# Optimization experiments

Measured on AMD Instinct MI355X. Metric: run time of the kernel, lower is better.

## Reference

```python
import jax, jax.numpy as jnp
import numpy as np

V, D, H, HD, L, T, B = 65, 384, 6, 64, 6, 256, 64
EPS = 1e-3  # keras LayerNormalization default epsilon


def setup_inputs() -> dict:
    key = jax.random.key(0)
    ks = jax.random.split(key, 12)
    s = 0.02
    n = lambda k, shp: jax.random.normal(k, shp, dtype=jnp.float32) * s
    return {
        "idx": jax.random.randint(ks[0], (B, T), 0, V),
        "tok_emb": n(ks[1], (V, D)),
        "pos_emb": n(ks[2], (T, D)),
        "Wq": n(ks[3], (L, H, D, HD)),
        "Wk": n(ks[4], (L, H, D, HD)),
        "Wv": n(ks[5], (L, H, D, HD)),
        "Wproj": n(ks[6], (L, D, D)),
        "bproj": jnp.zeros((L, D), jnp.float32),
        "W1": n(ks[7], (L, D, 4 * D)),
        "b1": jnp.zeros((L, 4 * D), jnp.float32),
        "W2": n(ks[8], (L, 4 * D, D)),
        "b2": jnp.zeros((L, D), jnp.float32),
        "ln1_g": jnp.ones((L, D), jnp.float32),
        "ln1_b": jnp.zeros((L, D), jnp.float32),
        "ln2_g": jnp.ones((L, D), jnp.float32),
        "ln2_b": jnp.zeros((L, D), jnp.float32),
        "lnf_g": jnp.ones((D,), jnp.float32),
        "lnf_b": jnp.zeros((D,), jnp.float32),
        "Whead": n(ks[9], (D, V)),
        "bhead": jnp.zeros((V,), jnp.float32),
    }


def _ln(x, g, b):
    m = jnp.mean(x, axis=-1, keepdims=True)
    v = jnp.mean(jnp.square(x - m), axis=-1, keepdims=True)
    return (x - m) * jax.lax.rsqrt(v + EPS) * g + b


def reference(idx, tok_emb, pos_emb, Wq, Wk, Wv, Wproj, bproj, W1, b1, W2, b2,
              ln1_g, ln1_b, ln2_g, ln2_b, lnf_g, lnf_b, Whead, bhead):
    Bn, Tn = idx.shape
    x = tok_emb[idx] + pos_emb[:Tn]  # [B,T,D]
    mask = jnp.tril(jnp.ones((Tn, Tn), dtype=bool))
    scale = jnp.float32(D) ** -0.5  # NOTE: original scales by full C=n_embd, not head_size
    for l in range(L):
        h = _ln(x, ln1_g[l], ln1_b[l])
        q = jnp.einsum('btd,hdk->bhtk', h, Wq[l])
        k = jnp.einsum('btd,hdk->bhtk', h, Wk[l])
        v = jnp.einsum('btd,hdk->bhtk', h, Wv[l])
        wei = jnp.einsum('bhtk,bhsk->bhts', q, k) * scale
        wei = jnp.where(mask, wei, -jnp.inf)
        wei = jax.nn.softmax(wei, axis=-1)
        att = jnp.einsum('bhts,bhsk->bhtk', wei, v)
        att = att.transpose(0, 2, 1, 3).reshape(Bn, Tn, D)  # concat heads
        x = x + att @ Wproj[l] + bproj[l]
        h2 = _ln(x, ln2_g[l], ln2_b[l])
        x = x + jax.nn.relu(h2 @ W1[l] + b1[l]) @ W2[l] + b2[l]
    x = _ln(x, lnf_g, lnf_b)
    return x @ Whead + bhead  # logits [B,T,V]
```

## Files before the change

kernel.cpp:

```cpp
#include <hip/hip_runtime.h>
#include <hip/hip_bf16.h>

#define B_  64
#define T_  256
#define D_  384
#define H_  6
#define HD_ 64
#define L_  6
#define V_  65
#define BT  (B_*T_)

typedef __hip_bfloat16 bf16;
typedef unsigned short u16;
typedef short s16;
typedef __attribute__((ext_vector_type(8))) short bf16x8;
typedef __attribute__((ext_vector_type(4))) float f32x4;

#define OFF_QKV   0
#define OFF_PROJ  442368
#define OFF_W1T   589824
#define OFF_W2T   1179648
#define OFF_BPROJ 1769472
#define OFF_B1    1769856
#define OFF_B2    1771392
#define OFF_LN1G  1771776
#define OFF_LN1B  1772160
#define OFF_LN2G  1772544
#define OFF_LN2B  1772928
#define WBUF_E    1773312
#define HOFF_WHT  0
#define HOFF_BH   24960
#define HOFF_LNFG 25088
#define HOFF_LNFB 25472
#define HBUF_E    25856

__device__ __forceinline__ float u2f(u16 u) {
  union { unsigned i; float f; } c; c.i = ((unsigned)u) << 16; return c.f;
}
__device__ __forceinline__ bf16 f2b(float x) { return __float2bfloat16(x); }
__device__ __forceinline__ float b2f(bf16 x) { return __bfloat162float(x); }
__device__ __forceinline__ u16 f2u(float x) { bf16 h = f2b(x); return *(u16*)&h; }

__device__ __forceinline__ float pload(const void* p, size_t i, bool f32w) {
  return f32w ? ((const float*)p)[i] : u2f(((const u16*)p)[i]);
}

__device__ __forceinline__ void swz(int gid, int ntc, int mtiles,
                                    int& nt, int& mblk) {
  if ((mtiles & 7) == 0) {
    int per = ntc << 3;
    int g   = gid / per;
    int rem = gid - g * per;
    nt   = rem >> 3;
    mblk = (g << 3) + (rem & 7);
  } else {
    nt   = gid / mtiles;
    mblk = gid - nt * mtiles;
  }
}

__global__ __launch_bounds__(256) void detect_kernel(
    const void* p1,  const void* p2,  const void* p3,  const void* p4,
    const void* p5,  const void* p6,  const void* p7,  const void* p8,
    const void* p9,  const void* p10, const void* p11, const void* p12,
    const void* p13, const void* p14, const void* p15, const void* p16,
    const void* p17, const void* p18, const void* p19,
    const int* __restrict__ idx, unsigned* flags)
{
  const void* ps[20] = {nullptr, p1, p2, p3, p4, p5, p6, p7, p8, p9, p10,
                        p11, p12, p13, p14, p15, p16, p17, p18, p19};
  const int esz[20] = {16384, 24960, 98304, 884736, 884736, 884736, 884736,
                       2304, 3538944, 9216, 3538944, 2304, 2304, 2304, 2304,
                       2304, 384, 384, 24960, 65};
  __shared__ int r1[256], r2[256];
  int bid = blockIdx.x, tid = threadIdx.x;
  if (bid == 19) {
    int z = 0;
    for (int m = tid; m < 4096; m += 256) z += (idx[2 * m + 1] == 0) ? 1 : 0;
    r1[tid] = z; __syncthreads();
    for (int s = 128; s > 0; s >>= 1) {
      if (tid < s) r1[tid] += r1[tid + s];
      __syncthreads();
    }
    if (tid == 0) flags[20] = (r1[0] >= 4000) ? 1u : 0u;
    return;
  }
  int j = bid + 1;
  const u16* p = (const u16*)ps[j];
  int ns = esz[j] / 2; if (ns > 1024) ns = 1024;
  int band = 0, nz = 0;
  for (int i = tid; i < ns; i += 256) {
    u16 lo = p[2 * i], hi = p[2 * i + 1];
    int e = (lo >> 7) & 0xFF;
    band += (e >= 100 && e <= 127) ? 1 : 0;
    nz   += (lo | hi) ? 1 : 0;
  }
  r1[tid] = band; r2[tid] = nz; __syncthreads();
  for (int s = 128; s > 0; s >>= 1) {
    if (tid < s) { r1[tid] += r1[tid + s]; r2[tid] += r2[tid + s]; }
    __syncthreads();
  }
  if (tid == 0) flags[j] = (r2[0] > 0 && r1[0] * 2 < ns) ? 1u : 0u;
}

__global__ void const_kernel(float* out, int n, float val) {
  int i = blockIdx.x * 256 + threadIdx.x;
  if (i < n) out[i] = val;
}

__global__ __launch_bounds__(256) void conv_layer(
    const void* Wq, const void* Wk, const void* Wv, const void* Wproj,
    const void* bproj, const void* W1, const void* b1, const void* W2,
    const void* b2, const void* ln1g, const void* ln1b, const void* ln2g,
    const void* ln2b, const unsigned* __restrict__ flags,
    bf16* __restrict__ dst, int l)
{
  int e = blockIdx.x * 256 + threadIdx.x;
  if (e >= WBUF_E) return;
  float v;
  if (e < OFF_PROJ) {
    int math = e / 24576;
    int rem  = e - math * 24576;
    int hd = rem / 384, d = rem - hd * 384;
    int mat = math / 6, hh = math - mat * 6;
    const void* src = (mat == 0 ? Wq : mat == 1 ? Wk : Wv);
    v = pload(src, ((size_t)(l * 6 + hh) * 384 + d) * 64 + hd, flags[3 + mat] != 0);
  } else if (e < OFF_W1T) {
    int e2 = e - OFF_PROJ;
    int n = e2 / 384, d = e2 - n * 384;
    v = pload(Wproj, ((size_t)l * 384 + d) * 384 + n, flags[6] != 0);
  } else if (e < OFF_W2T) {
    int e2 = e - OFF_W1T;
    int n = e2 / 384, d = e2 - n * 384;
    v = pload(W1, ((size_t)l * 384 + d) * 1536 + n, flags[8] != 0);
  } else if (e < OFF_BPROJ) {
    int e2 = e - OFF_W2T;
    int n = e2 / 1536, k = e2 - n * 1536;
    v = pload(W2, ((size_t)l * 1536 + k) * 384 + n, flags[10] != 0);
  } else {
    int e2 = e - OFF_BPROJ;
    if      (e2 < 384)  v = pload(bproj, (size_t)l * 384 + e2, flags[7] != 0);
    else if (e2 < 1920) v = pload(b1, (size_t)l * 1536 + (e2 - 384), flags[9] != 0);
    else if (e2 < 2304) v = pload(b2, (size_t)l * 384 + (e2 - 1920), flags[11] != 0);
    else if (e2 < 2688) v = pload(ln1g, (size_t)l * 384 + (e2 - 2304), flags[12] != 0);
    else if (e2 < 3072) v = pload(ln1b, (size_t)l * 384 + (e2 - 2688), flags[13] != 0);
    else if (e2 < 3456) v = pload(ln2g, (size_t)l * 384 + (e2 - 3072), flags[14] != 0);
    else                v = pload(ln2b, (size_t)l * 384 + (e2 - 3456), flags[15] != 0);
  }
  dst[e] = f2b(v);
}

__global__ __launch_bounds__(256) void conv_head(
    const void* Wh, const void* bh, const void* lnfg, const void* lnfb,
    const unsigned* __restrict__ flags, bf16* __restrict__ dst)
{
  int e = blockIdx.x * 256 + threadIdx.x;
  if (e >= HBUF_E) return;
  float v = 0.f;
  if (e < HOFF_BH) {
    int n = e / 384, d = e - n * 384;
    v = pload(Wh, (size_t)d * 65 + n, flags[18] != 0);
  } else if (e < 25025) {
    v = pload(bh, e - HOFF_BH, flags[19] != 0);
  } else if (e < HOFF_LNFG) {
    v = 0.f;
  } else if (e < HOFF_LNFB) {
    v = pload(lnfg, e - HOFF_LNFG, flags[16] != 0);
  } else {
    v = pload(lnfb, e - HOFF_LNFB, flags[17] != 0);
  }
  dst[e] = f2b(v);
}

__global__ __launch_bounds__(256) void embed_kernel(
    const void* __restrict__ idx, const void* __restrict__ tok,
    const void* __restrict__ pos, bf16* __restrict__ x,
    const unsigned* __restrict__ flags)
{
  int i   = blockIdx.x * 256 + threadIdx.x;
  int tkn = i / D_;
  int d   = i - tkn * D_;
  int t   = tkn & (T_ - 1);
  long long tix;
  if (flags[20]) tix = ((const long long*)idx)[tkn];
  else           tix = ((const int*)idx)[tkn];
  float v = pload(tok, (size_t)tix * D_ + d, flags[1] != 0)
          + pload(pos, (size_t)t * D_ + d, flags[2] != 0);
  x[i] = f2b(v);
}

__global__ __launch_bounds__(256) void lnw_kernel(
    const bf16* __restrict__ x, const u16* __restrict__ g,
    const u16* __restrict__ b, bf16* __restrict__ hc, int tok0)
{
  int w = threadIdx.x >> 6, lane = threadIdx.x & 63;
  int lm = blockIdx.x * 4 + w;
  const bf16* xr = x + (size_t)(tok0 + lm) * D_;
  float v[6]; float s = 0.f;
#pragma unroll
  for (int j = 0; j < 6; j++) { v[j] = b2f(xr[lane + 64 * j]); s += v[j]; }
#pragma unroll
  for (int o = 1; o < 64; o <<= 1) s += __shfl_xor(s, o, 64);
  float mean = s * (1.0f / D_);
  float sq = 0.f;
#pragma unroll
  for (int j = 0; j < 6; j++) { float d0 = v[j] - mean; sq += d0 * d0; }
#pragma unroll
  for (int o = 1; o < 64; o <<= 1) sq += __shfl_xor(sq, o, 64);
  float inv = 1.0f / sqrtf(sq * (1.0f / D_) + 1e-3f);
  bf16* hr = hc + (size_t)lm * D_;
#pragma unroll
  for (int j = 0; j < 6; j++) {
    int d = lane + 64 * j;
    hr[d] = f2b((v[j] - mean) * inv * u2f(g[d]) + u2f(b[d]));
  }
}

#define XS_S 72
#define WT_S 72

template<int RELU, int RESID, int OUTF32, int BIAS>
__device__ __forceinline__ void mgemm_core(
    s16* __restrict__ Xs, s16* __restrict__ Wt,
    const u16* __restrict__ A,
    const u16* __restrict__ WT, const bf16* __restrict__ bias,
    const bf16* __restrict__ resid, void* __restrict__ Cout,
    int ldC, int N, int K, int arow0, int crow0, int n0)
{
  int tid = threadIdx.x;
  int w = tid >> 6, lane = tid & 63;
  int quad = lane >> 4, l15 = lane & 15;
  f32x4 acc[2][4];
#pragma unroll
  for (int i = 0; i < 2; i++)
#pragma unroll
    for (int j = 0; j < 4; j++) acc[i][j] = (f32x4){0.f, 0.f, 0.f, 0.f};

  int xr = tid >> 1, xc = (tid & 1) * 32;
  int wn = tid >> 2, wk = (tid & 3) * 16;
  const u16* Ap0 = A + (size_t)(arow0 + xr) * K + xc;
  bool wvalid = (n0 + wn) < N;
  const u16* Wp0 = WT + (size_t)(wvalid ? (n0 + wn) : 0) * K + wk;

  for (int k0 = 0; k0 < K; k0 += 64) {
    bf16x8 xv[4];
#pragma unroll
    for (int i = 0; i < 4; i++) xv[i] = *(const bf16x8*)(Ap0 + k0 + 8 * i);
    bf16x8 wv[2];
#pragma unroll
    for (int i = 0; i < 2; i++)
      wv[i] = wvalid ? *(const bf16x8*)(Wp0 + k0 + 8 * i)
                     : (bf16x8){0,0,0,0,0,0,0,0};
    __syncthreads();
#pragma unroll
    for (int i = 0; i < 4; i++)
      *(bf16x8*)&Xs[xr * XS_S + xc + 8 * i] = xv[i];
#pragma unroll
    for (int i = 0; i < 2; i++)
      *(bf16x8*)&Wt[wn * WT_S + wk + 8 * i] = wv[i];
    __syncthreads();
#pragma unroll
    for (int kh = 0; kh < 2; kh++) {
      int kk = kh * 32 + quad * 8;
      bf16x8 a0 = *(const bf16x8*)&Xs[(w * 32 + l15) * XS_S + kk];
      bf16x8 a1 = *(const bf16x8*)&Xs[(w * 32 + 16 + l15) * XS_S + kk];
#pragma unroll
      for (int nt = 0; nt < 4; nt++) {
        bf16x8 b = *(const bf16x8*)&Wt[(nt * 16 + l15) * WT_S + kk];
        acc[0][nt] = __builtin_amdgcn_mfma_f32_16x16x32_bf16(a0, b, acc[0][nt], 0, 0, 0);
        acc[1][nt] = __builtin_amdgcn_mfma_f32_16x16x32_bf16(a1, b, acc[1][nt], 0, 0, 0);
      }
    }
  }

#pragma unroll
  for (int sub = 0; sub < 2; sub++)
#pragma unroll
    for (int nt = 0; nt < 4; nt++)
#pragma unroll
      for (int r = 0; r < 4; r++) {
        int m = w * 32 + sub * 16 + quad * 4 + r;
        int n = n0 + nt * 16 + l15;
        if (n < N) {
          float v = acc[sub][nt][r];
          if (BIAS)  v += b2f(bias[n]);
          if (RESID) v += b2f(resid[(size_t)(crow0 + m) * ldC + n]);
          if (RELU)  v = fmaxf(v, 0.f);
          if (OUTF32) ((float*)Cout)[(size_t)(crow0 + m) * ldC + n] = v;
          else        ((bf16*)Cout)[(size_t)(crow0 + m) * ldC + n]  = f2b(v);
        }
      }
}

#define MGEMM_LDS __shared__ s16 Xs[128 * XS_S]; __shared__ s16 Wt[64 * WT_S];

__global__ __launch_bounds__(256) void proj_mfma(
    const bf16* A, const bf16* Wbuf, bf16* x, int tok0, int mtiles)
{
  MGEMM_LDS
  int nt, mblk;
  swz(blockIdx.x, 6, mtiles, nt, mblk);
  int n0 = nt * 64, m0 = mblk * 128;
  mgemm_core<0,1,0,1>(Xs, Wt, (const u16*)A,
                      (const u16*)Wbuf + OFF_PROJ, (const bf16*)Wbuf + OFF_BPROJ,
                      x, x, D_, D_, D_, m0, tok0 + m0, n0);
}

__global__ __launch_bounds__(256) void ffn2_mfma(
    const bf16* midc, const bf16* Wbuf, bf16* x, int tok0, int mtiles)
{
  MGEMM_LDS
  int nt, mblk;
  swz(blockIdx.x, 6, mtiles, nt, mblk);
  int n0 = nt * 64, m0 = mblk * 128;
  mgemm_core<0,1,0,1>(Xs, Wt, (const u16*)midc,
                      (const u16*)Wbuf + OFF_W2T, (const bf16*)Wbuf + OFF_B2,
                      x, x, D_, D_, 4 * D_, m0, tok0 + m0, n0);
}

__global__ __launch_bounds__(256) void head_mfma(
    const bf16* hc, const bf16* Hbuf, float* out, int tok0)
{
  MGEMM_LDS
  int n0 = blockIdx.x * 64, m0 = blockIdx.y * 128;
  mgemm_core<0,0,1,1>(Xs, Wt, (const u16*)hc,
                      (const u16*)Hbuf + HOFF_WHT, (const bf16*)Hbuf + HOFF_BH,
                      nullptr, out, V_, V_, D_, m0, tok0 + m0, n0);
}

template<class Epi>
__device__ __forceinline__ void mg128(
    s16* __restrict__ Xs, s16* __restrict__ Ws,
    const u16* __restrict__ A,
    const u16* __restrict__ WT, int N, int K, int arow0, int n0, Epi epi)
{
  int tid = threadIdx.x;
  int w = tid >> 6, lane = tid & 63;
  int quad = lane >> 4, l15 = lane & 15;
  int wm = (w >> 1) * 64, wn = (w & 1) * 64;
  f32x4 acc[4][4];
#pragma unroll
  for (int i = 0; i < 4; i++)
#pragma unroll
    for (int j = 0; j < 4; j++) acc[i][j] = (f32x4){0.f, 0.f, 0.f, 0.f};

  int sr = tid >> 1, sc = (tid & 1) * 32;
  const u16* Ap0 = A + (size_t)(arow0 + sr) * K + sc;
  bool nv = (n0 + sr) < N;
  const u16* Wp0 = WT + (size_t)(nv ? (n0 + sr) : 0) * K + sc;

  for (int k0 = 0; k0 < K; k0 += 64) {
    bf16x8 xv[4], wv[4];
#pragma unroll
    for (int i = 0; i < 4; i++) xv[i] = *(const bf16x8*)(Ap0 + k0 + 8 * i);
#pragma unroll
    for (int i = 0; i < 4; i++)
      wv[i] = nv ? *(const bf16x8*)(Wp0 + k0 + 8 * i)
                 : (bf16x8){0,0,0,0,0,0,0,0};
    __syncthreads();
#pragma unroll
    for (int i = 0; i < 4; i++) {
      *(bf16x8*)&Xs[sr * 72 + sc + 8 * i] = xv[i];
      *(bf16x8*)&Ws[sr * 72 + sc + 8 * i] = wv[i];
    }
    __syncthreads();
#pragma unroll
    for (int kh = 0; kh < 2; kh++) {
      int kk = kh * 32 + quad * 8;
      bf16x8 am[4], bn[4];
#pragma unroll
      for (int i = 0; i < 4; i++)
        am[i] = *(const bf16x8*)&Xs[(wm + i * 16 + l15) * 72 + kk];
#pragma unroll
      for (int j = 0; j < 4; j++)
        bn[j] = *(const bf16x8*)&Ws[(wn + j * 16 + l15) * 72 + kk];
#pragma unroll
      for (int i = 0; i < 4; i++)
#pragma unroll
        for (int j = 0; j < 4; j++)
          acc[i][j] = __builtin_amdgcn_mfma_f32_16x16x32_bf16(am[i], bn[j], acc[i][j], 0, 0, 0);
    }
  }

#pragma unroll
  for (int i = 0; i < 4; i++)
#pragma unroll
    for (int j = 0; j < 4; j++)
#pragma unroll
      for (int r = 0; r < 4; r++) {
        int m = wm + i * 16 + quad * 4 + r;
        int n = n0 + wn + j * 16 + l15;
        if (n < N) epi(m, n, acc[i][j][r]);
      }
}

#define MG128_LDS __shared__ s16 Xs[128 * 72]; __shared__ s16 Ws[128 * 72];

__global__ __launch_bounds__(256) void qkv128(
    const bf16* hc, const bf16* Wbuf, bf16* qkvc, int MCa, int mtiles)
{
  MG128_LDS
  int nt, mblk;
  swz(blockIdx.x, 9, mtiles, nt, mblk);
  int n0 = nt * 128, mloc0 = mblk * 128;
  auto epi = [&](int m, int n, float v) {
    int mat = n / 384;
    int rem = n - mat * 384;
    int hh = rem >> 6, hd = rem & 63;
    qkvc[(size_t)mat * MCa * D_ + (size_t)hh * MCa * HD_
         + (size_t)(mloc0 + m) * HD_ + hd] = f2b(v);
  };
  mg128(Xs, Ws, (const u16*)hc,
        (const u16*)Wbuf + OFF_QKV, 1152, D_, mloc0, n0, epi);
}

__global__ __launch_bounds__(256) void ffn1_128(
    const bf16* hc, const bf16* Wbuf, bf16* midc, int mtiles)
{
  MG128_LDS
  int nt, mblk;
  swz(blockIdx.x, 12, mtiles, nt, mblk);
  int n0 = nt * 128, m0 = mblk * 128;
  const bf16* bias = (const bf16*)Wbuf + OFF_B1;
  auto epi = [&](int m, int n, float v) {
    float r = v + b2f(bias[n]);
    midc[(size_t)(m0 + m) * (4 * D_) + n] = f2b(fmaxf(r, 0.f));
  };
  mg128(Xs, Ws, (const u16*)hc,
        (const u16*)Wbuf + OFF_W1T, 4 * D_, D_, m0, n0, epi);
}

__global__ __launch_bounds__(256) void attn4_kernel(
    const bf16* __restrict__ Q, const bf16* __restrict__ K,
    const bf16* __restrict__ V, bf16* __restrict__ att, int MCa)
{
  __shared__ s16 Qs[64 * 72];
  __shared__ s16 Ks[64 * 72];
  __shared__ s16 Vs[64 * 73];
  __shared__ s16 Ps[4][16 * 72];
  const float scale = 0.05103103630798288f;
  int tid = threadIdx.x;
  int w = tid >> 6, lane = tid & 63;
  int quad = lane >> 4, l15 = lane & 15;
  int bid = blockIdx.x;
  int qt = bid & 3;
  int bh = bid >> 2;
  int b = bh / H_, h = bh - b * H_;
  size_t base = ((size_t)h * MCa + (size_t)b * T_) * HD_;
  int q0 = qt * 64;
  int cq = qt;

#pragma unroll
  for (int i = 0; i < 2; i++) {
    int e = i * 256 + tid;
    int r = e >> 3, c = (e & 7) * 8;
    *(bf16x8*)&Qs[r * 72 + c] =
        *(const bf16x8*)((const u16*)Q + base + (size_t)(q0 + r) * HD_ + c);
  }

  float mrow[4] = {-1e30f, -1e30f, -1e30f, -1e30f};
  float lrow[4] = {0.f, 0.f, 0.f, 0.f};
  f32x4 O[4];
#pragma unroll
  for (int nt = 0; nt < 4; nt++) O[nt] = (f32x4){0.f, 0.f, 0.f, 0.f};

  for (int c = 0; c <= cq; c++) {
    __syncthreads();
#pragma unroll
    for (int i = 0; i < 2; i++) {
      int e = i * 256 + tid;
      int r = e >> 3, cc = (e & 7) * 8;
      *(bf16x8*)&Ks[r * 72 + cc] =
          *(const bf16x8*)((const u16*)K + base + (size_t)(c * 64 + r) * HD_ + cc);
      bf16x8 vv =
          *(const bf16x8*)((const u16*)V + base + (size_t)(c * 64 + r) * HD_ + cc);
#pragma unroll
      for (int k = 0; k < 8; k++) Vs[r * 73 + cc + k] = vv[k];
    }
    __syncthreads();

    f32x4 S[4];
#pragma unroll
    for (int nt = 0; nt < 4; nt++) S[nt] = (f32x4){0.f, 0.f, 0.f, 0.f};
#pragma unroll
    for (int ks = 0; ks < 2; ks++) {
      int kk = ks * 32 + quad * 8;
      bf16x8 a = *(const bf16x8*)&Qs[(w * 16 + l15) * 72 + kk];
#pragma unroll
      for (int nt = 0; nt < 4; nt++) {
        bf16x8 bb8 = *(const bf16x8*)&Ks[(nt * 16 + l15) * 72 + kk];
        S[nt] = __builtin_amdgcn_mfma_f32_16x16x32_bf16(a, bb8, S[nt], 0, 0, 0);
      }
    }

#pragma unroll
    for (int nt = 0; nt < 4; nt++)
#pragma unroll
      for (int r = 0; r < 4; r++) {
        int qrow = q0 + w * 16 + quad * 4 + r;
        int sg = c * 64 + nt * 16 + l15;
        float v = S[nt][r] * scale;
        S[nt][r] = (sg <= qrow) ? v : -1e30f;
      }

    float alpha[4];
#pragma unroll
    for (int r = 0; r < 4; r++) {
      float mc = fmaxf(fmaxf(S[0][r], S[1][r]), fmaxf(S[2][r], S[3][r]));
#pragma unroll
      for (int o = 1; o < 16; o <<= 1) mc = fmaxf(mc, __shfl_xor(mc, o, 64));
      float mn = fmaxf(mrow[r], mc);
      alpha[r] = __expf(mrow[r] - mn);
      mrow[r] = mn;
      float s = 0.f;
#pragma unroll
      for (int nt = 0; nt < 4; nt++) {
        float p = __expf(S[nt][r] - mn);
        S[nt][r] = p;
        s += p;
      }
#pragma unroll
      for (int o = 1; o < 16; o <<= 1) s += __shfl_xor(s, o, 64);
      lrow[r] = lrow[r] * alpha[r] + s;
    }
#pragma unroll
    for (int nt = 0; nt < 4; nt++)
#pragma unroll
      for (int r = 0; r < 4; r++) O[nt][r] *= alpha[r];

#pragma unroll
    for (int nt = 0; nt < 4; nt++)
#pragma unroll
      for (int r = 0; r < 4; r++)
        Ps[w][(quad * 4 + r) * 72 + nt * 16 + l15] = (s16)f2u(S[nt][r]);
    __syncthreads();
#pragma unroll
    for (int ks = 0; ks < 2; ks++) {
      bf16x8 a = *(const bf16x8*)&Ps[w][l15 * 72 + ks * 32 + quad * 8];
#pragma unroll
      for (int nt = 0; nt < 4; nt++) {
        bf16x8 bb8;
#pragma unroll
        for (int j = 0; j < 8; j++)
          bb8[j] = Vs[(ks * 32 + quad * 8 + j) * 73 + nt * 16 + l15];
        O[nt] = __builtin_amdgcn_mfma_f32_16x16x32_bf16(a, bb8, O[nt], 0, 0, 0);
      }
    }
  }

#pragma unroll
  for (int r = 0; r < 4; r++) {
    float invl = 1.0f / lrow[r];
#pragma unroll
    for (int nt = 0; nt < 4; nt++) {
      int qrow = q0 + w * 16 + quad * 4 + r;
      att[(size_t)(b * T_ + qrow) * D_ + h * HD_ + nt * 16 + l15] =
          f2b(O[nt][r] * invl);
    }
  }
}

extern "C" void kernel_launch(void* const* d_in, const int* in_sizes, int n_in,
                              void* d_out, int out_size, void* d_ws, size_t ws_size,
                              hipStream_t stream)
{
  float* out = (float*)d_out;
  dim3 blk(256);
  int outg = (out_size + 255) / 256;

  static const int expected[20] = {
      16384, 24960, 98304, 884736, 884736, 884736, 884736, 2304,
      3538944, 9216, 3538944, 2304, 2304, 2304, 2304, 2304, 384, 384,
      24960, 65};
  if (n_in != 20) { const_kernel<<<outg, blk, 0, stream>>>(out, out_size, 5.0f); return; }
  for (int i = 0; i < 20; i++)
    if (in_sizes[i] != expected[i]) {
      const_kernel<<<outg, blk, 0, stream>>>(out, out_size, 10.0f * (i + 1));
      return;
    }
  if (out_size != BT * V_) { const_kernel<<<outg, blk, 0, stream>>>(out, out_size, 7.0f); return; }

  const void* idx   = d_in[0];
  const void* tok   = d_in[1];
  const void* pos   = d_in[2];
  const void* Wq    = d_in[3];
  const void* Wk    = d_in[4];
  const void* Wv    = d_in[5];
  const void* Wproj = d_in[6];
  const void* bproj = d_in[7];
  const void* W1    = d_in[8];
  const void* b1    = d_in[9];
  const void* W2    = d_in[10];
  const void* b2    = d_in[11];
  const void* ln1g  = d_in[12];
  const void* ln1b  = d_in[13];
  const void* ln2g  = d_in[14];
  const void* ln2b  = d_in[15];
  const void* lnfg  = d_in[16];
  const void* lnfb  = d_in[17];
  const void* Whead = d_in[18];
  const void* bhead = d_in[19];

  const size_t off_x  = 256;
  const size_t off_wb = off_x + (size_t)BT * D_ * 2;
  const size_t off_hb = off_wb + (size_t)WBUF_E * 2;
  const size_t fixed  = off_hb + ((size_t)HBUF_E * 2 + 63) / 64 * 64;
  if (ws_size < fixed) {
    const_kernel<<<outg, blk, 0, stream>>>(out, out_size, 0.0f);
    return;
  }
  size_t region = ws_size - fixed;

  int nc = 0;
  const int candn[7] = {1, 2, 4, 8, 16, 32, 64};
  for (int i = 0; i < 7; i++)
    if ((size_t)5 * (BT / candn[i]) * D_ * 2 <= region) { nc = candn[i]; break; }
  if (!nc) { const_kernel<<<outg, blk, 0, stream>>>(out, out_size, 0.0f); return; }
  const int MCc = BT / nc;
  const int CBc = MCc / T_;
  const int mtiles = MCc / 128;

  char* wsb = (char*)d_ws;
  unsigned* flags = (unsigned*)wsb;
  bf16*   x    = (bf16*)(wsb + off_x);
  bf16*   Wbuf = (bf16*)(wsb + off_wb);
  bf16*   Hbuf = (bf16*)(wsb + off_hb);
  bf16*   hc   = (bf16*)(wsb + fixed);
  bf16*   qkvc = hc + (size_t)MCc * D_;
  bf16*   attc = qkvc + (size_t)3 * MCc * D_;
  bf16*   midc = qkvc;

  detect_kernel<<<dim3(20), blk, 0, stream>>>(
      tok, pos, Wq, Wk, Wv, Wproj, bproj, W1, b1, W2, b2,
      ln1g, ln1b, ln2g, ln2b, lnfg, lnfb, Whead, bhead,
      (const int*)idx, flags);
  embed_kernel<<<dim3(BT * D_ / 256), blk, 0, stream>>>(idx, tok, pos, x, flags);
  conv_head<<<dim3((HBUF_E + 255) / 256), blk, 0, stream>>>(
      Whead, bhead, lnfg, lnfb, flags, Hbuf);

  for (int l = 0; l < L_; l++) {
    conv_layer<<<dim3((WBUF_E + 255) / 256), blk, 0, stream>>>(
        Wq, Wk, Wv, Wproj, bproj, W1, b1, W2, b2,
        ln1g, ln1b, ln2g, ln2b, flags, Wbuf, l);
    for (int c = 0; c < nc; c++) {
      int tok0 = c * MCc;
      lnw_kernel<<<dim3(MCc / 4), blk, 0, stream>>>(
          x, (const u16*)Wbuf + OFF_LN1G, (const u16*)Wbuf + OFF_LN1B, hc, tok0);
      qkv128<<<dim3(9 * mtiles), blk, 0, stream>>>(hc, Wbuf, qkvc, MCc, mtiles);
      attn4_kernel<<<dim3(CBc * H_ * 4), blk, 0, stream>>>(
          qkvc, qkvc + (size_t)MCc * D_, qkvc + (size_t)2 * MCc * D_, attc, MCc);
      proj_mfma<<<dim3(6 * mtiles), blk, 0, stream>>>(attc, Wbuf, x, tok0, mtiles);
    }
    for (int f = 0; f < nc; f++) {
      int tok0 = f * MCc;
      lnw_kernel<<<dim3(MCc / 4), blk, 0, stream>>>(
          x, (const u16*)Wbuf + OFF_LN2G, (const u16*)Wbuf + OFF_LN2B, hc, tok0);
      ffn1_128<<<dim3(12 * mtiles), blk, 0, stream>>>(hc, Wbuf, midc, mtiles);
      ffn2_mfma<<<dim3(6 * mtiles), blk, 0, stream>>>(midc, Wbuf, x, tok0, mtiles);
    }
  }

  for (int c = 0; c < nc; c++) {
    int tok0 = c * MCc;
    lnw_kernel<<<dim3(MCc / 4), blk, 0, stream>>>(
        x, (const u16*)Hbuf + HOFF_LNFG, (const u16*)Hbuf + HOFF_LNFB, hc, tok0);
    head_mfma<<<dim3(2, MCc / 128), blk, 0, stream>>>(hc, Hbuf, out, tok0);
  }
}
```

Measured before the change: 1.276 ms.

## Load GEMM tiles directly into LDS with XOR-swizzled layout via global_load_lds

```diff
diff --git a/kernel.cpp b/kernel.cpp
--- a/kernel.cpp
+++ b/kernel.cpp
@@ -216,166 +216,67 @@
   }
 }
 
-#define XS_S 72
-#define WT_S 72
-
-template<int RELU, int RESID, int OUTF32, int BIAS>
-__device__ __forceinline__ void mgemm_core(
-    s16* __restrict__ Xs, s16* __restrict__ Wt,
-    const u16* __restrict__ A,
-    const u16* __restrict__ WT, const bf16* __restrict__ bias,
-    const bf16* __restrict__ resid, void* __restrict__ Cout,
-    int ldC, int N, int K, int arow0, int crow0, int n0)
-{
+__device__ __forceinline__ void gll16(const void* g, void* l) {
+  __builtin_amdgcn_global_load_lds(
+      (const __attribute__((address_space(1))) unsigned*)g,
+      (__attribute__((address_space(3))) unsigned*)l, 16, 0, 0);
+}
+
+__device__ __forceinline__ bf16x8 ldfrag(const s16* lds, int r, int s) {
+  return *(const bf16x8*)(lds + r * 64 + ((s ^ (r & 7)) << 3));
+}
+
+template<int NT, class Epi>
+__device__ __forceinline__ void mcore(
+    s16* __restrict__ As, s16* __restrict__ Wl,
+    const u16* __restrict__ A, const u16* __restrict__ WT,
+    int N, int K, int arow0, int n0, Epi epi)
+{
+  constexpr int MREP = (NT == 128) ? 4 : 2;
+  constexpr int WPW  = NT / 32;
   int tid = threadIdx.x;
   int w = tid >> 6, lane = tid & 63;
   int quad = lane >> 4, l15 = lane & 15;
-  f32x4 acc[2][4];
-#pragma unroll
-  for (int i = 0; i < 2; i++)
+  int r8 = lane >> 3;
+  int sl = ((lane & 7) ^ r8) * 8;
+  int wm = (NT == 128) ? ((w >> 1) * 64) : (w * 32);
+  int wn = (NT == 128) ? ((w & 1) * 64) : 0;
+
+  f32x4 acc[MREP][4];
+#pragma unroll
+  for (int i = 0; i < MREP; i++)
 #pragma unroll
     for (int j = 0; j < 4; j++) acc[i][j] = (f32x4){0.f, 0.f, 0.f, 0.f};
 
-  int xr = tid >> 1, xc = (tid & 1) * 32;
-  int wn = tid >> 2, wk = (tid & 3) * 16;
-  const u16* Ap0 = A + (size_t)(arow0 + xr) * K + xc;
-  bool wvalid = (n0 + wn) < N;
-  const u16* Wp0 = WT + (size_t)(wvalid ? (n0 + wn) : 0) * K + wk;
+  const u16* Ag[4];
+#pragma unroll
+  for (int i = 0; i < 4; i++)
+    Ag[i] = A + (size_t)(arow0 + (w * 4 + i) * 8 + r8) * K + sl;
+  const u16* Wg[WPW];
+#pragma unroll
+  for (int i = 0; i < WPW; i++)
+    Wg[i] = WT + (size_t)(n0 + (w * WPW + i) * 8 + r8) * K + sl;
 
   for (int k0 = 0; k0 < K; k0 += 64) {
-    bf16x8 xv[4];
-#pragma unroll
-    for (int i = 0; i < 4; i++) xv[i] = *(const bf16x8*)(Ap0 + k0 + 8 * i);
-    bf16x8 wv[2];
-#pragma unroll
-    for (int i = 0; i < 2; i++)
-      wv[i] = wvalid ? *(const bf16x8*)(Wp0 + k0 + 8 * i)
-                     : (bf16x8){0,0,0,0,0,0,0,0};
     __syncthreads();
 #pragma unroll
     for (int i = 0; i < 4; i++)
-      *(bf16x8*)&Xs[xr * XS_S + xc + 8 * i] = xv[i];
-#pragma unroll
-    for (int i = 0; i < 2; i++)
-      *(bf16x8*)&Wt[wn * WT_S + wk + 8 * i] = wv[i];
+      gll16(Ag[i] + k0, As + (w * 4 + i) * 512);
+#pragma unroll
+    for (int i = 0; i < WPW; i++)
+      gll16(Wg[i] + k0, Wl + (w * WPW + i) * 512);
     __syncthreads();
 #pragma unroll
     for (int kh = 0; kh < 2; kh++) {
-      int kk = kh * 32 + quad * 8;
-      bf16x8 a0 = *(const bf16x8*)&Xs[(w * 32 + l15) * XS_S + kk];
-      bf16x8 a1 = *(const bf16x8*)&Xs[(w * 32 + 16 + l15) * XS_S + kk];
-#pragma unroll
-      for (int nt = 0; nt < 4; nt++) {
-        bf16x8 b = *(const bf16x8*)&Wt[(nt * 16 + l15) * WT_S + kk];
-        acc[0][nt] = __builtin_amdgcn_mfma_f32_16x16x32_bf16(a0, b, acc[0][nt], 0, 0, 0);
-        acc[1][nt] = __builtin_amdgcn_mfma_f32_16x16x32_bf16(a1, b, acc[1][nt], 0, 0, 0);
-      }
-    }
-  }
-
-#pragma unroll
-  for (int sub = 0; sub < 2; sub++)
-#pragma unroll
-    for (int nt = 0; nt < 4; nt++)
-#pragma unroll
-      for (int r = 0; r < 4; r++) {
-        int m = w * 32 + sub * 16 + quad * 4 + r;
-        int n = n0 + nt * 16 + l15;
-        if (n < N) {
-          float v = acc[sub][nt][r];
-          if (BIAS)  v += b2f(bias[n]);
-          if (RESID) v += b2f(resid[(size_t)(crow0 + m) * ldC + n]);
-          if (RELU)  v = fmaxf(v, 0.f);
-          if (OUTF32) ((float*)Cout)[(size_t)(crow0 + m) * ldC + n] = v;
-          else        ((bf16*)Cout)[(size_t)(crow0 + m) * ldC + n]  = f2b(v);
-        }
-      }
-}
-
-#define MGEMM_LDS __shared__ s16 Xs[128 * XS_S]; __shared__ s16 Wt[64 * WT_S];
-
-__global__ __launch_bounds__(256) void proj_mfma(
-    const bf16* A, const bf16* Wbuf, bf16* x, int tok0, int mtiles)
-{
-  MGEMM_LDS
-  int nt, mblk;
-  swz(blockIdx.x, 6, mtiles, nt, mblk);
-  int n0 = nt * 64, m0 = mblk * 128;
-  mgemm_core<0,1,0,1>(Xs, Wt, (const u16*)A,
-                      (const u16*)Wbuf + OFF_PROJ, (const bf16*)Wbuf + OFF_BPROJ,
-                      x, x, D_, D_, D_, m0, tok0 + m0, n0);
-}
-
-__global__ __launch_bounds__(256) void ffn2_mfma(
-    const bf16* midc, const bf16* Wbuf, bf16* x, int tok0, int mtiles)
-{
-  MGEMM_LDS
-  int nt, mblk;
-  swz(blockIdx.x, 6, mtiles, nt, mblk);
-  int n0 = nt * 64, m0 = mblk * 128;
-  mgemm_core<0,1,0,1>(Xs, Wt, (const u16*)midc,
-                      (const u16*)Wbuf + OFF_W2T, (const bf16*)Wbuf + OFF_B2,
-                      x, x, D_, D_, 4 * D_, m0, tok0 + m0, n0);
-}
-
-__global__ __launch_bounds__(256) void head_mfma(
-    const bf16* hc, const bf16* Hbuf, float* out, int tok0)
-{
-  MGEMM_LDS
-  int n0 = blockIdx.x * 64, m0 = blockIdx.y * 128;
-  mgemm_core<0,0,1,1>(Xs, Wt, (const u16*)hc,
-                      (const u16*)Hbuf + HOFF_WHT, (const bf16*)Hbuf + HOFF_BH,
-                      nullptr, out, V_, V_, D_, m0, tok0 + m0, n0);
-}
-
-template<class Epi>
-__device__ __forceinline__ void mg128(
-    s16* __restrict__ Xs, s16* __restrict__ Ws,
-    const u16* __restrict__ A,
-    const u16* __restrict__ WT, int N, int K, int arow0, int n0, Epi epi)
-{
-  int tid = threadIdx.x;
-  int w = tid >> 6, lane = tid & 63;
-  int quad = lane >> 4, l15 = lane & 15;
-  int wm = (w >> 1) * 64, wn = (w & 1) * 64;
-  f32x4 acc[4][4];
-#pragma unroll
-  for (int i = 0; i < 4; i++)
-#pragma unroll
-    for (int j = 0; j < 4; j++) acc[i][j] = (f32x4){0.f, 0.f, 0.f, 0.f};
-
-  int sr = tid >> 1, sc = (tid & 1) * 32;
-  const u16* Ap0 = A + (size_t)(arow0 + sr) * K + sc;
-  bool nv = (n0 + sr) < N;
-  const u16* Wp0 = WT + (size_t)(nv ? (n0 + sr) : 0) * K + sc;
-
-  for (int k0 = 0; k0 < K; k0 += 64) {
-    bf16x8 xv[4], wv[4];
-#pragma unroll
-    for (int i = 0; i < 4; i++) xv[i] = *(const bf16x8*)(Ap0 + k0 + 8 * i);
-#pragma unroll
-    for (int i = 0; i < 4; i++)
-      wv[i] = nv ? *(const bf16x8*)(Wp0 + k0 + 8 * i)
-                 : (bf16x8){0,0,0,0,0,0,0,0};
-    __syncthreads();
-#pragma unroll
-    for (int i = 0; i < 4; i++) {
-      *(bf16x8*)&Xs[sr * 72 + sc + 8 * i] = xv[i];
-      *(bf16x8*)&Ws[sr * 72 + sc + 8 * i] = wv[i];
-    }
-    __syncthreads();
-#pragma unroll
-    for (int kh = 0; kh < 2; kh++) {
-      int kk = kh * 32 + quad * 8;
-      bf16x8 am[4], bn[4];
-#pragma unroll
-      for (int i = 0; i < 4; i++)
-        am[i] = *(const bf16x8*)&Xs[(wm + i * 16 + l15) * 72 + kk];
+      bf16x8 am[MREP], bn[4];
+#pragma unroll
+      for (int i = 0; i < MREP; i++)
+        am[i] = ldfrag(As, wm + i * 16 + l15, kh * 4 + quad);
 #pragma unroll
       for (int j = 0; j < 4; j++)
-        bn[j] = *(const bf16x8*)&Ws[(wn + j * 16 + l15) * 72 + kk];
-#pragma unroll
-      for (int i = 0; i < 4; i++)
+        bn[j] = ldfrag(Wl, wn + j * 16 + l15, kh * 4 + quad);
+#pragma unroll
+      for (int i = 0; i < MREP; i++)
 #pragma unroll
         for (int j = 0; j < 4; j++)
           acc[i][j] = __builtin_amdgcn_mfma_f32_16x16x32_bf16(am[i], bn[j], acc[i][j], 0, 0, 0);
@@ -383,7 +284,7 @@
   }
 
 #pragma unroll
-  for (int i = 0; i < 4; i++)
+  for (int i = 0; i < MREP; i++)
 #pragma unroll
     for (int j = 0; j < 4; j++)
 #pragma unroll
@@ -394,12 +295,11 @@
       }
 }
 
-#define MG128_LDS __shared__ s16 Xs[128 * 72]; __shared__ s16 Ws[128 * 72];
-
 __global__ __launch_bounds__(256) void qkv128(
     const bf16* hc, const bf16* Wbuf, bf16* qkvc, int MCa, int mtiles)
 {
-  MG128_LDS
+  __shared__ __attribute__((aligned(16))) s16 As[128 * 64];
+  __shared__ __attribute__((aligned(16))) s16 Ws[128 * 64];
   int nt, mblk;
   swz(blockIdx.x, 9, mtiles, nt, mblk);
   int n0 = nt * 128, mloc0 = mblk * 128;
@@ -410,14 +310,15 @@
     qkvc[(size_t)mat * MCa * D_ + (size_t)hh * MCa * HD_
          + (size_t)(mloc0 + m) * HD_ + hd] = f2b(v);
   };
-  mg128(Xs, Ws, (const u16*)hc,
-        (const u16*)Wbuf + OFF_QKV, 1152, D_, mloc0, n0, epi);
+  mcore<128>(As, Ws, (const u16*)hc,
+             (const u16*)Wbuf + OFF_QKV, 1152, D_, mloc0, n0, epi);
 }
 
 __global__ __launch_bounds__(256) void ffn1_128(
     const bf16* hc, const bf16* Wbuf, bf16* midc, int mtiles)
 {
-  MG128_LDS
+  __shared__ __attribute__((aligned(16))) s16 As[128 * 64];
+  __shared__ __attribute__((aligned(16))) s16 Ws[128 * 64];
   int nt, mblk;
   swz(blockIdx.x, 12, mtiles, nt, mblk);
   int n0 = nt * 128, m0 = mblk * 128;
@@ -426,8 +327,56 @@
     float r = v + b2f(bias[n]);
     midc[(size_t)(m0 + m) * (4 * D_) + n] = f2b(fmaxf(r, 0.f));
   };
-  mg128(Xs, Ws, (const u16*)hc,
-        (const u16*)Wbuf + OFF_W1T, 4 * D_, D_, m0, n0, epi);
+  mcore<128>(As, Ws, (const u16*)hc,
+             (const u16*)Wbuf + OFF_W1T, 4 * D_, D_, m0, n0, epi);
+}
+
+__global__ __launch_bounds__(256) void proj_mfma(
+    const bf16* A, const bf16* Wbuf, bf16* x, int tok0, int mtiles)
+{
+  __shared__ __attribute__((aligned(16))) s16 As[128 * 64];
+  __shared__ __attribute__((aligned(16))) s16 Ws[64 * 64];
+  int nt, mblk;
+  swz(blockIdx.x, 6, mtiles, nt, mblk);
+  int n0 = nt * 64, m0 = mblk * 128;
+  const bf16* bias = (const bf16*)Wbuf + OFF_BPROJ;
+  auto epi = [&](int m, int n, float v) {
+    size_t o = (size_t)(tok0 + m0 + m) * D_ + n;
+    x[o] = f2b(v + b2f(bias[n]) + b2f(x[o]));
+  };
+  mcore<64>(As, Ws, (const u16*)A,
+            (const u16*)Wbuf + OFF_PROJ, D_, D_, m0, n0, epi);
+}
+
+__global__ __launch_bounds__(256) void ffn2_mfma(
+    const bf16* midc, const bf16* Wbuf, bf16* x, int tok0, int mtiles)
+{
+  __shared__ __attribute__((aligned(16))) s16 As[128 * 64];
+  __shared__ __attribute__((aligned(16))) s16 Ws[64 * 64];
+  int nt, mblk;
+  swz(blockIdx.x, 6, mtiles, nt, mblk);
+  int n0 = nt * 64, m0 = mblk * 128;
+  const bf16* bias = (const bf16*)Wbuf + OFF_B2;
+  auto epi = [&](int m, int n, float v) {
+    size_t o = (size_t)(tok0 + m0 + m) * D_ + n;
+    x[o] = f2b(v + b2f(bias[n]) + b2f(x[o]));
+  };
+  mcore<64>(As, Ws, (const u16*)midc,
+            (const u16*)Wbuf + OFF_W2T, D_, 4 * D_, m0, n0, epi);
+}
+
+__global__ __launch_bounds__(256) void head_mfma(
+    const bf16* hc, const bf16* Hbuf, float* out, int tok0)
+{
+  __shared__ __attribute__((aligned(16))) s16 As[128 * 64];
+  __shared__ __attribute__((aligned(16))) s16 Ws[64 * 64];
+  int n0 = blockIdx.x * 64, m0 = blockIdx.y * 128;
+  const bf16* bias = (const bf16*)Hbuf + HOFF_BH;
+  auto epi = [&](int m, int n, float v) {
+    out[(size_t)(tok0 + m0 + m) * V_ + n] = v + b2f(bias[n]);
+  };
+  mcore<64>(As, Ws, (const u16*)hc,
+            (const u16*)Hbuf + HOFF_WHT, V_, D_, m0, n0, epi);
 }
 
 __global__ __launch_bounds__(256) void attn4_kernel(
```

After: 1.194 ms. 1.07x faster.
